# Performance work log

Measured on AMD Instinct MI355X. Metric: run time of the kernel, lower is better.

The kernel has to match this reference:

```python
import jax, jax.numpy as jnp
import numpy as np

EPS = 0.01  # Normalizer eps
N_NODES = 100000
N_EDGES = 1600000


def gcn_conv(x, edge_index, W, b, n_nodes):
    """PyG-style GCNConv: x @ W, symmetric-normalized aggregation with self-loops, + bias."""
    src = jnp.concatenate([edge_index[0], jnp.arange(n_nodes)])  # [E+N]
    dst = jnp.concatenate([edge_index[1], jnp.arange(n_nodes)])  # [E+N]
    h = x @ W  # [N, out]
    ones = jnp.ones_like(dst, dtype=h.dtype)
    deg = jax.ops.segment_sum(ones, dst, num_segments=n_nodes)  # [N]
    dinv = jnp.where(deg > 0, jax.lax.rsqrt(deg), 0.0)
    norm = dinv[src] * dinv[dst]  # [E+N]
    msgs = h[src] * norm[:, None]  # [E+N, out]  (largest intermediate)
    out = jax.ops.segment_sum(msgs, dst, num_segments=n_nodes)  # [N, out]
    return out + b


def setup_inputs() -> dict:
    key = jax.random.key(0)
    k = jax.random.split(key, 6)
    x = jax.random.normal(k[0], (N_NODES, 16), dtype=jnp.float32)
    edge_index = jax.random.randint(k[1], (2, N_EDGES), 0, N_NODES)
    W1 = jax.random.normal(k[2], (16, 64), dtype=jnp.float32) * 0.25
    b1 = jax.random.normal(k[3], (64,), dtype=jnp.float32) * 0.1
    W3 = jax.random.normal(k[4], (64, 32), dtype=jnp.float32) * 0.125
    b3 = jax.random.normal(k[5], (32,), dtype=jnp.float32) * 0.1
    return {"x": x, "edge_index": edge_index, "W1": W1, "b1": b1, "W3": W3, "b3": b3}


def reference(x, edge_index, W1, b1, W3, b3):
    n = x.shape[0]
    h = jax.nn.relu(gcn_conv(x, edge_index, W1, b1, n))
    h = jax.nn.relu(gcn_conv(h, edge_index, W3, b3, n))
    # Normalizer: sequential Welford observe over all nodes then normalize with
    # FINAL stats == population mean / clamped population variance.
    mean = h.mean(axis=0)  # [32]
    var = jnp.maximum(((h - mean) ** 2).mean(axis=0), EPS)  # [32]
    return (h - mean) * jax.lax.rsqrt(var)
```

## Files before the change

### kernel.cpp

```cpp
#include <hip/hip_runtime.h>
#include <hip/hip_fp16.h>

#define EPS 0.01f
#define SCAN_BS 512
#define NCHUNKS 256
#define BUCKET_SHIFT 9
#define BUCKET_SZ (1 << BUCKET_SHIFT)
#define STAGE_CAP 16384


__global__ __launch_bounds__(SCAN_BS) void k_scan_block(const int* __restrict__ in,
                                                        int* __restrict__ out,
                                                        int* __restrict__ bsum, int n) {
    __shared__ int sd[SCAN_BS];
    int t = threadIdx.x;
    int gid = blockIdx.x * SCAN_BS + t;
    int v = (gid < n) ? in[gid] : 0;
    sd[t] = v;
    __syncthreads();
    for (int off = 1; off < SCAN_BS; off <<= 1) {
        int x = (t >= off) ? sd[t - off] : 0;
        __syncthreads();
        sd[t] += x;
        __syncthreads();
    }
    if (gid < n) out[gid] = sd[t] - v;
    if (t == SCAN_BS - 1) bsum[blockIdx.x] = sd[t];
}

__global__ __launch_bounds__(SCAN_BS) void k_scan_tops(int* __restrict__ bsum, int nb) {
    __shared__ int sd[SCAN_BS];
    int t = threadIdx.x;
    int v = (t < nb) ? bsum[t] : 0;
    sd[t] = v;
    __syncthreads();
    for (int off = 1; off < SCAN_BS; off <<= 1) {
        int x = (t >= off) ? sd[t - off] : 0;
        __syncthreads();
        sd[t] += x;
        __syncthreads();
    }
    if (t < nb) bsum[t] = sd[t] - v;
}

__global__ __launch_bounds__(SCAN_BS) void k_scan_add(int* __restrict__ out,
                                                      const int* __restrict__ bsum, int n) {
    int gid = blockIdx.x * SCAN_BS + threadIdx.x;
    if (gid < n) out[gid] += bsum[blockIdx.x];
}


__global__ __launch_bounds__(256) void kA_bucket_hist(const int* __restrict__ dst,
                                                      int* __restrict__ bh, int e,
                                                      int nbuck, int ce) {
    extern __shared__ int hist[];
    int b = blockIdx.x, t = threadIdx.x;
    for (int i = t; i < nbuck; i += 256) hist[i] = 0;
    __syncthreads();
    int lo = b * ce, hi = min(lo + ce, e);
    for (int i = lo + t; i < hi; i += 256) atomicAdd(&hist[dst[i] >> BUCKET_SHIFT], 1);
    __syncthreads();
    for (int i = t; i < nbuck; i += 256) bh[i * NCHUNKS + b] = hist[i];
}

__global__ __launch_bounds__(256) void kC_bucket_scatter(const int* __restrict__ src,
                                                         const int* __restrict__ dst,
                                                         const int* __restrict__ bhs,
                                                         unsigned int* __restrict__ eb, int e,
                                                         int nbuck, int ce) {
    extern __shared__ int cur[];
    int b = blockIdx.x, t = threadIdx.x;
    for (int i = t; i < nbuck; i += 256) cur[i] = bhs[i * NCHUNKS + b];
    __syncthreads();
    int lo = b * ce, hi = min(lo + ce, e);
    for (int i = lo + t; i < hi; i += 256) {
        int s = src[i], d = dst[i];
        int pos = atomicAdd(&cur[d >> BUCKET_SHIFT], 1);
        eb[pos] = ((unsigned int)(d & (BUCKET_SZ - 1)) << 23) | (unsigned int)s;
    }
}

__global__ __launch_bounds__(256) void kDeg_fill_prescale(const unsigned int* __restrict__ eb,
                                                          const int* __restrict__ bhs,
                                                          const float* __restrict__ x,
                                                          int* __restrict__ degi,
                                                          float* __restrict__ dinv,
                                                          int* __restrict__ rowstart,
                                                          int* __restrict__ csr_src,
                                                          __half* __restrict__ xs,
                                                          float* __restrict__ partial,
                                                          int n, int nbuck, int e) {
    __shared__ unsigned int ebs[STAGE_CAP];
    __shared__ int hist[BUCKET_SZ];
    __shared__ int ps[256];
    __shared__ float dv[BUCKET_SZ];
    int k = blockIdx.x, t = threadIdx.x;
    if (k == 0 && t < 64) partial[t] = 0.f;
    for (int i = t; i < BUCKET_SZ; i += 256) hist[i] = 0;
    __syncthreads();
    int lo = bhs[k * NCHUNKS];
    int hi = (k + 1 < nbuck) ? bhs[(k + 1) * NCHUNKS] : e;
    int cnt = hi - lo;
    bool fits = (cnt <= STAGE_CAP);
    for (int i = t; i < cnt; i += 256) {
        unsigned int p = eb[lo + i];
        if (fits) ebs[i] = p;
        atomicAdd(&hist[p >> 23], 1);
    }
    __syncthreads();
    int a0 = hist[2 * t], a1 = hist[2 * t + 1];
    ps[t] = a0 + a1;
    __syncthreads();
    for (int off = 1; off < 256; off <<= 1) {
        int v = (t >= off) ? ps[t - off] : 0;
        __syncthreads();
        ps[t] += v;
        __syncthreads();
    }
    int excl = ps[t] - (a0 + a1);
    int node0 = k << BUCKET_SHIFT;
    int rs0 = lo + excl, rs1 = lo + excl + a0;
    {
        int nd0 = node0 + 2 * t, nd1 = nd0 + 1;
        float d0 = rsqrtf((float)a0 + 1.0f);
        float d1 = rsqrtf((float)a1 + 1.0f);
        dv[2 * t] = d0;
        dv[2 * t + 1] = d1;
        if (nd0 < n) {
            degi[nd0] = a0;
            dinv[nd0] = d0;
            rowstart[nd0] = rs0;
        }
        if (nd1 < n) {
            degi[nd1] = a1;
            dinv[nd1] = d1;
            rowstart[nd1] = rs1;
        }
    }
    __syncthreads();
    hist[2 * t] = rs0;
    hist[2 * t + 1] = rs1;
    {
        const float2* xf2 = (const float2*)x;
        __half2* xs2 = (__half2*)xs;
        for (int i = t; i < BUCKET_SZ * 8; i += 256) {
            int rl = i >> 3;
            int node = node0 + rl;
            if (node < n) {
                float2 vv = xf2[(size_t)node * 8 + (i & 7)];
                float d = dv[rl];
                xs2[(size_t)node * 8 + (i & 7)] = __floats2half2_rn(vv.x * d, vv.y * d);
            }
        }
    }
    __syncthreads();
    for (int i = t; i < cnt; i += 256) {
        unsigned int p = fits ? ebs[i] : eb[lo + i];
        int dl = (int)(p >> 23);
        int s = (int)(p & 0x7fffffu);
        int pos = atomicAdd(&hist[dl], 1);
        csr_src[pos] = s;
    }
}


__global__ __launch_bounds__(256) void k_l1_fused(const int* __restrict__ rowstart,
                                                  const int* __restrict__ degi,
                                                  const int* __restrict__ csr_src,
                                                  const float* __restrict__ dinv,
                                                  const __half* __restrict__ xs,
                                                  const float* __restrict__ W1,
                                                  const float* __restrict__ b1,
                                                  const float* __restrict__ W3,
                                                  __half* __restrict__ h2sA,
                                                  __half* __restrict__ h2sB, int n) {
    __shared__ float w1[16 * 64];
    __shared__ float w3[64 * 32];
    __shared__ float bs[64];
    __shared__ __align__(16) float a[16 * 16];
    __shared__ float z[16 * 64];
    int t = threadIdx.x;
    for (int i = t; i < 16 * 64; i += 256) w1[i] = W1[i];
    for (int i = t; i < 64 * 32; i += 256) w3[i] = W3[i];
    if (t < 64) bs[t] = b1[t];

    int row0 = blockIdx.x * 16;
    int wv = t >> 6;
    int lane = t & 63;
    int c2 = lane & 3;
    int slot = lane >> 2;
    const float2* xf2 = (const float2*)xs;

    for (int nid = 0; nid < 4; ++nid) {
        int node = row0 + wv * 4 + nid;
        if (node < n) {
            const int* sp = csr_src + rowstart[node];
            int deg = degi[node];
            int L = (deg + 15) >> 4;
            int base = slot * L;
            int end = min(base + L, deg);
            __half2 acc0 = __float2half2_rn(0.f), acc1 = acc0;
            for (int k = base; k < end; ++k) {
                int s0 = sp[k];
                float2 raw = xf2[(size_t)s0 * 4 + c2];
                acc0 = __hadd2(acc0, *(const __half2*)&raw.x);
                acc1 = __hadd2(acc1, *(const __half2*)&raw.y);
            }
#pragma unroll
            for (int m = 4; m <= 32; m <<= 1) {
                float o0 = __shfl_xor(*(float*)&acc0, m);
                float o1 = __shfl_xor(*(float*)&acc1, m);
                acc0 = __hadd2(acc0, *(__half2*)&o0);
                acc1 = __hadd2(acc1, *(__half2*)&o1);
            }
            if (slot == 0) {
                float2 lo = __half22float2(acc0), hi = __half22float2(acc1);
                float2 sraw = xf2[(size_t)node * 4 + c2];
                float2 slo = __half22float2(*(const __half2*)&sraw.x);
                float2 shi = __half22float2(*(const __half2*)&sraw.y);
                float dn = dinv[node];
                int r = wv * 4 + nid;
                float4 res;
                res.x = dn * (lo.x + slo.x);
                res.y = dn * (lo.y + slo.y);
                res.z = dn * (hi.x + shi.x);
                res.w = dn * (hi.y + shi.y);
                ((float4*)(a + r * 16))[c2] = res;
            }
        }
    }
    __syncthreads();

    for (int i = t; i < 1024; i += 256) {
        int r = i >> 6, c = i & 63;
        float acc = bs[c];
#pragma unroll
        for (int k = 0; k < 16; ++k) acc += a[r * 16 + k] * w1[k * 64 + c];
        z[i] = acc > 0.f ? acc : 0.f;
    }
    __syncthreads();
    for (int i = t; i < 512; i += 256) {
        int r = i >> 5, c = i & 31;
        float acc = 0.f;
#pragma unroll
        for (int k = 0; k < 64; ++k) acc += z[r * 64 + k] * w3[k * 32 + c];
        int row = row0 + r;
        if (row < n) {
            __half hv = __float2half(acc * dinv[row]);
            if (c < 16) h2sA[(size_t)row * 16 + c] = hv;
            else        h2sB[(size_t)row * 16 + (c - 16)] = hv;
        }
    }
}


__global__ __launch_bounds__(256) void k_gather16x2_stats(const int* __restrict__ rowstart,
                                                          const int* __restrict__ degi,
                                                          const int* __restrict__ csr_src,
                                                          const float* __restrict__ dinv,
                                                          const __half* __restrict__ h2sA,
                                                          const __half* __restrict__ h2sB,
                                                          const float* __restrict__ b3,
                                                          float* __restrict__ out,
                                                          float* __restrict__ partial, int n) {
    int g = blockIdx.x;
    int half = (g >> 2) & 1;
    int nblk = (g >> 3) * 4 + (g & 3);
    int M = (n + 31) >> 5;
    if (nblk >= M) return;
    const float2* h2f = (const float2*)(half ? h2sB : h2sA);
    int col0 = half << 4;
    int t = threadIdx.x;
    int lane = t & 63;
    int c2 = lane & 3;
    int slot = lane >> 2;
    int wv = t >> 6;
    float4 bias = ((const float4*)(b3 + col0))[c2];
    float4 sacc = make_float4(0.f, 0.f, 0.f, 0.f);
    float4 qacc = make_float4(0.f, 0.f, 0.f, 0.f);
    for (int it = 0; it < 8; ++it) {
        int node = nblk * 32 + it * 4 + wv;
        if (node < n) {
            const int* sp = csr_src + rowstart[node];
            int deg = degi[node];
            int L = (deg + 15) >> 4;
            int base = slot * L;
            int end = min(base + L, deg);
            __half2 acc0 = __float2half2_rn(0.f), acc1 = acc0;
            for (int k = base; k < end; ++k) {
                int s0 = sp[k];
                float2 raw = h2f[(size_t)s0 * 4 + c2];
                acc0 = __hadd2(acc0, *(const __half2*)&raw.x);
                acc1 = __hadd2(acc1, *(const __half2*)&raw.y);
            }
#pragma unroll
            for (int m = 4; m <= 32; m <<= 1) {
                float o0 = __shfl_xor(*(float*)&acc0, m);
                float o1 = __shfl_xor(*(float*)&acc1, m);
                acc0 = __hadd2(acc0, *(__half2*)&o0);
                acc1 = __hadd2(acc1, *(__half2*)&o1);
            }
            if (slot == 0) {
                float2 lo = __half22float2(acc0), hi = __half22float2(acc1);
                float2 sraw = h2f[(size_t)node * 4 + c2];
                float2 slo = __half22float2(*(const __half2*)&sraw.x);
                float2 shi = __half22float2(*(const __half2*)&sraw.y);
                float dn = dinv[node];
                float4 v;
                v.x = dn * (lo.x + slo.x) + bias.x;
                v.y = dn * (lo.y + slo.y) + bias.y;
                v.z = dn * (hi.x + shi.x) + bias.z;
                v.w = dn * (hi.y + shi.y) + bias.w;
                v.x = fmaxf(v.x, 0.f);
                v.y = fmaxf(v.y, 0.f);
                v.z = fmaxf(v.z, 0.f);
                v.w = fmaxf(v.w, 0.f);
                ((float4*)(out + (size_t)node * 32 + col0))[c2] = v;
                sacc.x += v.x; sacc.y += v.y; sacc.z += v.z; sacc.w += v.w;
                qacc.x += v.x * v.x; qacc.y += v.y * v.y;
                qacc.z += v.z * v.z; qacc.w += v.w * v.w;
            }
        }
    }
    __shared__ __align__(16) float ls[64], lq[64];
    if (slot == 0) {
        ((float4*)ls)[wv * 4 + c2] = sacc;
        ((float4*)lq)[wv * 4 + c2] = qacc;
    }
    __syncthreads();
    if (t < 16) {
        float a = 0.f, b = 0.f;
#pragma unroll
        for (int w = 0; w < 4; ++w) {
            a += ls[w * 16 + t];
            b += lq[w * 16 + t];
        }
        atomicAdd(&partial[col0 + t], a);
        atomicAdd(&partial[32 + col0 + t], b);
    }
}


__global__ void k_finalize(const float* __restrict__ partial, float* __restrict__ meaninv, int n) {
    int t = threadIdx.x;
    if (t < 32) {
        float invn = 1.0f / (float)n;
        float mean = partial[t] * invn;
        float var = partial[32 + t] * invn - mean * mean;
        var = var > EPS ? var : EPS;
        meaninv[t] = mean;
        meaninv[32 + t] = rsqrtf(var);
    }
}

__global__ void k_norm(float* __restrict__ h, const float* __restrict__ meaninv, int n) {
    int idx = blockIdx.x * blockDim.x + threadIdx.x;
    if (idx < n * 8) {
        int c4 = idx & 7;
        float4 v = ((float4*)h)[idx];
        float4 m = ((const float4*)meaninv)[c4];
        float4 iv = ((const float4*)(meaninv + 32))[c4];
        v.x = (v.x - m.x) * iv.x;
        v.y = (v.y - m.y) * iv.y;
        v.z = (v.z - m.z) * iv.z;
        v.w = (v.w - m.w) * iv.w;
        ((float4*)h)[idx] = v;
    }
}

extern "C" void kernel_launch(void* const* d_in, const int* in_sizes, int n_in,
                              void* d_out, int out_size, void* d_ws, size_t ws_size,
                              hipStream_t stream) {
    const float* x  = (const float*)d_in[0];
    const int* ei   = (const int*)d_in[1];
    const float* W1 = (const float*)d_in[2];
    const float* b1 = (const float*)d_in[3];
    const float* W3 = (const float*)d_in[4];
    const float* b3 = (const float*)d_in[5];

    const int N = in_sizes[0] / 16;
    const int E = in_sizes[1] / 2;
    const int* src = ei;
    const int* dst = ei + E;

    const int NBUCK = (N + BUCKET_SZ - 1) >> BUCKET_SHIFT;
    const int CE = (E + NCHUNKS - 1) / NCHUNKS;
    const int BH_TOTAL = NBUCK * NCHUNKS;

    char* ws = (char*)d_ws;
    int*   degi     = (int*)ws;          ws += (size_t)N * 4;
    float* dinv     = (float*)ws;        ws += (size_t)N * 4;
    int*   rowstart = (int*)ws;          ws += (size_t)N * 4;
    int*   bsum2    = (int*)ws;          ws += (size_t)SCAN_BS * 4;
    int*   bh       = (int*)ws;          ws += (size_t)BH_TOTAL * 4;
    int*   bhs      = (int*)ws;          ws += (size_t)BH_TOTAL * 4;
    unsigned int* eb = (unsigned int*)ws; ws += (size_t)E * 4;
    int*   csr_src  = (int*)ws;          ws += (size_t)E * 4;
    __half* xs      = (__half*)ws;       ws += (size_t)N * 16 * 2;
    __half* h2sA    = (__half*)ws;       ws += (size_t)N * 16 * 2;
    __half* h2sB    = (__half*)ws;       ws += (size_t)N * 16 * 2;
    float* partial  = (float*)ws;        ws += 64 * 4;
    float* meaninv  = (float*)ws;

    float* out = (float*)d_out;

    const int NB2 = (BH_TOTAL + SCAN_BS - 1) / SCAN_BS;

    kA_bucket_hist<<<NCHUNKS, 256, NBUCK * 4, stream>>>(dst, bh, E, NBUCK, CE);
    k_scan_block<<<NB2, SCAN_BS, 0, stream>>>(bh, bhs, bsum2, BH_TOTAL);
    k_scan_tops<<<1, SCAN_BS, 0, stream>>>(bsum2, NB2);
    k_scan_add<<<NB2, SCAN_BS, 0, stream>>>(bhs, bsum2, BH_TOTAL);
    kC_bucket_scatter<<<NCHUNKS, 256, NBUCK * 4, stream>>>(src, dst, bhs, eb, E, NBUCK, CE);

    kDeg_fill_prescale<<<NBUCK, 256, 0, stream>>>(eb, bhs, x, degi, dinv, rowstart,
                                                  csr_src, xs, partial, N, NBUCK, E);

    k_l1_fused<<<(N + 15) / 16, 256, 0, stream>>>(rowstart, degi, csr_src, dinv, xs,
                                                  W1, b1, W3, h2sA, h2sB, N);

    const int M = (N + 31) >> 5;
    const int G = ((M + 3) / 4) * 8;
    k_gather16x2_stats<<<G, 256, 0, stream>>>(rowstart, degi, csr_src, dinv, h2sA, h2sB,
                                              b3, out, partial, N);

    k_finalize<<<1, 64, 0, stream>>>(partial, meaninv, N);
    k_norm<<<(N * 8 + 255) / 256, 256, 0, stream>>>(out, meaninv, N);
}
```

Measured before the change: 191.7 us.

## Batch neighbor gathers across nodes per wave and merge layer-2 column halves

Layer-1 and layer-2 gathers now have each wave process 4 or 8 nodes together. Every lane loads neighbour indices for all of those nodes up front, in a fixed number of unrolled rounds, so many independent loads are in flight instead of one serial loop per node. Accumulation moves from half2 to fp32. The layer-2 features are stored as a single 32-wide half array instead of two 16-wide halves, so one kernel gathers full 64-byte rows rather than launching separate column-half blocks. The cost is higher register pressure from the unrolled per-node accumulators and wasted lanes on low-degree nodes.

```diff
diff --git a/kernel.cpp b/kernel.cpp
--- a/kernel.cpp
+++ b/kernel.cpp
@@ -172,8 +172,7 @@
                                                   const float* __restrict__ W1,
                                                   const float* __restrict__ b1,
                                                   const float* __restrict__ W3,
-                                                  __half* __restrict__ h2sA,
-                                                  __half* __restrict__ h2sB, int n) {
+                                                  __half* __restrict__ h2s, int n) {
     __shared__ float w1[16 * 64];
     __shared__ float w3[64 * 32];
     __shared__ float bs[64];
@@ -187,156 +186,216 @@
     int row0 = blockIdx.x * 16;
     int wv = t >> 6;
     int lane = t & 63;
-    int c2 = lane & 3;
-    int slot = lane >> 2;
+    int g = lane >> 2;
+    int c = lane & 3;
+    int nb = row0 + wv * 4;
     const float2* xf2 = (const float2*)xs;
 
-    for (int nid = 0; nid < 4; ++nid) {
-        int node = row0 + wv * 4 + nid;
-        if (node < n) {
-            const int* sp = csr_src + rowstart[node];
-            int deg = degi[node];
-            int L = (deg + 15) >> 4;
-            int base = slot * L;
-            int end = min(base + L, deg);
-            __half2 acc0 = __float2half2_rn(0.f), acc1 = acc0;
-            for (int k = base; k < end; ++k) {
-                int s0 = sp[k];
-                float2 raw = xf2[(size_t)s0 * 4 + c2];
-                acc0 = __hadd2(acc0, *(const __half2*)&raw.x);
-                acc1 = __hadd2(acc1, *(const __half2*)&raw.y);
+    int rs[4], dg[4];
+#pragma unroll
+    for (int i = 0; i < 4; ++i) {
+        int nd = nb + i;
+        bool ok = nd < n;
+        rs[i] = ok ? rowstart[nd] : 0;
+        dg[i] = ok ? degi[nd] : 0;
+    }
+    float4 acc[4];
+#pragma unroll
+    for (int i = 0; i < 4; ++i) acc[i] = make_float4(0.f, 0.f, 0.f, 0.f);
+
+#pragma unroll
+    for (int r = 0; r < 2; ++r) {
+        int k = r * 16 + g;
+        int idx[4];
+#pragma unroll
+        for (int i = 0; i < 4; ++i) idx[i] = (k < dg[i]) ? csr_src[rs[i] + k] : -1;
+#pragma unroll
+        for (int i = 0; i < 4; ++i) {
+            if (idx[i] >= 0) {
+                float2 raw = xf2[(size_t)idx[i] * 4 + c];
+                float2 lo = __half22float2(*(const __half2*)&raw.x);
+                float2 hi = __half22float2(*(const __half2*)&raw.y);
+                acc[i].x += lo.x; acc[i].y += lo.y;
+                acc[i].z += hi.x; acc[i].w += hi.y;
             }
-#pragma unroll
-            for (int m = 4; m <= 32; m <<= 1) {
-                float o0 = __shfl_xor(*(float*)&acc0, m);
-                float o1 = __shfl_xor(*(float*)&acc1, m);
-                acc0 = __hadd2(acc0, *(__half2*)&o0);
-                acc1 = __hadd2(acc1, *(__half2*)&o1);
+        }
+    }
+#pragma unroll
+    for (int i = 0; i < 4; ++i) {
+        for (int k = 32 + g; k < dg[i]; k += 16) {
+            int s0 = csr_src[rs[i] + k];
+            float2 raw = xf2[(size_t)s0 * 4 + c];
+            float2 lo = __half22float2(*(const __half2*)&raw.x);
+            float2 hi = __half22float2(*(const __half2*)&raw.y);
+            acc[i].x += lo.x; acc[i].y += lo.y;
+            acc[i].z += hi.x; acc[i].w += hi.y;
+        }
+    }
+#pragma unroll
+    for (int i = 0; i < 4; ++i) {
+#pragma unroll
+        for (int m = 4; m <= 32; m <<= 1) {
+            acc[i].x += __shfl_xor(acc[i].x, m);
+            acc[i].y += __shfl_xor(acc[i].y, m);
+            acc[i].z += __shfl_xor(acc[i].z, m);
+            acc[i].w += __shfl_xor(acc[i].w, m);
+        }
+    }
+#pragma unroll
+    for (int i = 0; i < 4; ++i) {
+        int nd = nb + i;
+        if (g == i && nd < n) {
+            float dn = dinv[nd];
+            float2 sraw = xf2[(size_t)nd * 4 + c];
+            float2 slo = __half22float2(*(const __half2*)&sraw.x);
+            float2 shi = __half22float2(*(const __half2*)&sraw.y);
+            float4 res;
+            res.x = dn * (acc[i].x + slo.x);
+            res.y = dn * (acc[i].y + slo.y);
+            res.z = dn * (acc[i].z + shi.x);
+            res.w = dn * (acc[i].w + shi.y);
+            ((float4*)(a + (wv * 4 + i) * 16))[c] = res;
+        }
+    }
+    __syncthreads();
+
+    for (int i = t; i < 1024; i += 256) {
+        int r = i >> 6, cc = i & 63;
+        float acc2 = bs[cc];
+#pragma unroll
+        for (int k = 0; k < 16; ++k) acc2 += a[r * 16 + k] * w1[k * 64 + cc];
+        z[i] = acc2 > 0.f ? acc2 : 0.f;
+    }
+    __syncthreads();
+    for (int i = t; i < 512; i += 256) {
+        int r = i >> 5, cc = i & 31;
+        float acc2 = 0.f;
+#pragma unroll
+        for (int k = 0; k < 64; ++k) acc2 += z[r * 64 + k] * w3[k * 32 + cc];
+        int row = row0 + r;
+        if (row < n) h2s[(size_t)row * 32 + cc] = __float2half(acc2 * dinv[row]);
+    }
+}
+
+
+__global__ __launch_bounds__(256) void k_l2_stats(const int* __restrict__ rowstart,
+                                                  const int* __restrict__ degi,
+                                                  const int* __restrict__ csr_src,
+                                                  const float* __restrict__ dinv,
+                                                  const __half* __restrict__ h2s,
+                                                  const float* __restrict__ b3,
+                                                  float* __restrict__ out,
+                                                  float* __restrict__ partial, int n) {
+    int t = threadIdx.x;
+    int wv = t >> 6;
+    int lane = t & 63;
+    int g = lane >> 3;
+    int c = lane & 7;
+    int nb = blockIdx.x * 32 + wv * 8;
+    const float2* h2f = (const float2*)h2s;
+
+    int rs[8], dg[8];
+#pragma unroll
+    for (int i = 0; i < 8; ++i) {
+        int nd = nb + i;
+        bool ok = nd < n;
+        rs[i] = ok ? rowstart[nd] : 0;
+        dg[i] = ok ? degi[nd] : 0;
+    }
+    float4 acc[8];
+#pragma unroll
+    for (int i = 0; i < 8; ++i) acc[i] = make_float4(0.f, 0.f, 0.f, 0.f);
+
+#pragma unroll
+    for (int r = 0; r < 3; ++r) {
+        int k = r * 8 + g;
+        int idx[8];
+#pragma unroll
+        for (int i = 0; i < 8; ++i) idx[i] = (k < dg[i]) ? csr_src[rs[i] + k] : -1;
+#pragma unroll
+        for (int i = 0; i < 8; ++i) {
+            if (idx[i] >= 0) {
+                float2 raw = h2f[(size_t)idx[i] * 8 + c];
+                float2 lo = __half22float2(*(const __half2*)&raw.x);
+                float2 hi = __half22float2(*(const __half2*)&raw.y);
+                acc[i].x += lo.x; acc[i].y += lo.y;
+                acc[i].z += hi.x; acc[i].w += hi.y;
             }
-            if (slot == 0) {
-                float2 lo = __half22float2(acc0), hi = __half22float2(acc1);
-                float2 sraw = xf2[(size_t)node * 4 + c2];
-                float2 slo = __half22float2(*(const __half2*)&sraw.x);
-                float2 shi = __half22float2(*(const __half2*)&sraw.y);
-                float dn = dinv[node];
-                int r = wv * 4 + nid;
-                float4 res;
-                res.x = dn * (lo.x + slo.x);
-                res.y = dn * (lo.y + slo.y);
-                res.z = dn * (hi.x + shi.x);
-                res.w = dn * (hi.y + shi.y);
-                ((float4*)(a + r * 16))[c2] = res;
-            }
-        }
-    }
-    __syncthreads();
-
-    for (int i = t; i < 1024; i += 256) {
-        int r = i >> 6, c = i & 63;
-        float acc = bs[c];
-#pragma unroll
-        for (int k = 0; k < 16; ++k) acc += a[r * 16 + k] * w1[k * 64 + c];
-        z[i] = acc > 0.f ? acc : 0.f;
-    }
-    __syncthreads();
-    for (int i = t; i < 512; i += 256) {
-        int r = i >> 5, c = i & 31;
-        float acc = 0.f;
-#pragma unroll
-        for (int k = 0; k < 64; ++k) acc += z[r * 64 + k] * w3[k * 32 + c];
-        int row = row0 + r;
-        if (row < n) {
-            __half hv = __float2half(acc * dinv[row]);
-            if (c < 16) h2sA[(size_t)row * 16 + c] = hv;
-            else        h2sB[(size_t)row * 16 + (c - 16)] = hv;
-        }
-    }
-}
-
-
-__global__ __launch_bounds__(256) void k_gather16x2_stats(const int* __restrict__ rowstart,
-                                                          const int* __restrict__ degi,
-                                                          const int* __restrict__ csr_src,
-                                                          const float* __restrict__ dinv,
-                                                          const __half* __restrict__ h2sA,
-                                                          const __half* __restrict__ h2sB,
-                                                          const float* __restrict__ b3,
-                                                          float* __restrict__ out,
-                                                          float* __restrict__ partial, int n) {
-    int g = blockIdx.x;
-    int half = (g >> 2) & 1;
-    int nblk = (g >> 3) * 4 + (g & 3);
-    int M = (n + 31) >> 5;
-    if (nblk >= M) return;
-    const float2* h2f = (const float2*)(half ? h2sB : h2sA);
-    int col0 = half << 4;
-    int t = threadIdx.x;
-    int lane = t & 63;
-    int c2 = lane & 3;
-    int slot = lane >> 2;
-    int wv = t >> 6;
-    float4 bias = ((const float4*)(b3 + col0))[c2];
-    float4 sacc = make_float4(0.f, 0.f, 0.f, 0.f);
-    float4 qacc = make_float4(0.f, 0.f, 0.f, 0.f);
-    for (int it = 0; it < 8; ++it) {
-        int node = nblk * 32 + it * 4 + wv;
-        if (node < n) {
-            const int* sp = csr_src + rowstart[node];
-            int deg = degi[node];
-            int L = (deg + 15) >> 4;
-            int base = slot * L;
-            int end = min(base + L, deg);
-            __half2 acc0 = __float2half2_rn(0.f), acc1 = acc0;
-            for (int k = base; k < end; ++k) {
-                int s0 = sp[k];
-                float2 raw = h2f[(size_t)s0 * 4 + c2];
-                acc0 = __hadd2(acc0, *(const __half2*)&raw.x);
-                acc1 = __hadd2(acc1, *(const __half2*)&raw.y);
-            }
-#pragma unroll
-            for (int m = 4; m <= 32; m <<= 1) {
-                float o0 = __shfl_xor(*(float*)&acc0, m);
-                float o1 = __shfl_xor(*(float*)&acc1, m);
-                acc0 = __hadd2(acc0, *(__half2*)&o0);
-                acc1 = __hadd2(acc1, *(__half2*)&o1);
-            }
-            if (slot == 0) {
-                float2 lo = __half22float2(acc0), hi = __half22float2(acc1);
-                float2 sraw = h2f[(size_t)node * 4 + c2];
-                float2 slo = __half22float2(*(const __half2*)&sraw.x);
-                float2 shi = __half22float2(*(const __half2*)&sraw.y);
-                float dn = dinv[node];
-                float4 v;
-                v.x = dn * (lo.x + slo.x) + bias.x;
-                v.y = dn * (lo.y + slo.y) + bias.y;
-                v.z = dn * (hi.x + shi.x) + bias.z;
-                v.w = dn * (hi.y + shi.y) + bias.w;
-                v.x = fmaxf(v.x, 0.f);
-                v.y = fmaxf(v.y, 0.f);
-                v.z = fmaxf(v.z, 0.f);
-                v.w = fmaxf(v.w, 0.f);
-                ((float4*)(out + (size_t)node * 32 + col0))[c2] = v;
-                sacc.x += v.x; sacc.y += v.y; sacc.z += v.z; sacc.w += v.w;
-                qacc.x += v.x * v.x; qacc.y += v.y * v.y;
-                qacc.z += v.z * v.z; qacc.w += v.w * v.w;
-            }
-        }
-    }
-    __shared__ __align__(16) float ls[64], lq[64];
-    if (slot == 0) {
-        ((float4*)ls)[wv * 4 + c2] = sacc;
-        ((float4*)lq)[wv * 4 + c2] = qacc;
-    }
-    __syncthreads();
-    if (t < 16) {
-        float a = 0.f, b = 0.f;
+        }
+    }
+#pragma unroll
+    for (int i = 0; i < 8; ++i) {
+        for (int k = 24 + g; k < dg[i]; k += 8) {
+            int s0 = csr_src[rs[i] + k];
+            float2 raw = h2f[(size_t)s0 * 8 + c];
+            float2 lo = __half22float2(*(const __half2*)&raw.x);
+            float2 hi = __half22float2(*(const __half2*)&raw.y);
+            acc[i].x += lo.x; acc[i].y += lo.y;
+            acc[i].z += hi.x; acc[i].w += hi.y;
+        }
+    }
+#pragma unroll
+    for (int i = 0; i < 8; ++i) {
+#pragma unroll
+        for (int m = 8; m <= 32; m <<= 1) {
+            acc[i].x += __shfl_xor(acc[i].x, m);
+            acc[i].y += __shfl_xor(acc[i].y, m);
+            acc[i].z += __shfl_xor(acc[i].z, m);
+            acc[i].w += __shfl_xor(acc[i].w, m);
+        }
+    }
+    float4 s4 = make_float4(0.f, 0.f, 0.f, 0.f);
+    float4 q4 = make_float4(0.f, 0.f, 0.f, 0.f);
+    float4 bias = ((const float4*)b3)[c];
+#pragma unroll
+    for (int i = 0; i < 8; ++i) {
+        int nd = nb + i;
+        if (g == i && nd < n) {
+            float dn = dinv[nd];
+            float2 sraw = h2f[(size_t)nd * 8 + c];
+            float2 slo = __half22float2(*(const __half2*)&sraw.x);
+            float2 shi = __half22float2(*(const __half2*)&sraw.y);
+            float4 v;
+            v.x = fmaxf(dn * (acc[i].x + slo.x) + bias.x, 0.f);
+            v.y = fmaxf(dn * (acc[i].y + slo.y) + bias.y, 0.f);
+            v.z = fmaxf(dn * (acc[i].z + shi.x) + bias.z, 0.f);
+            v.w = fmaxf(dn * (acc[i].w + shi.y) + bias.w, 0.f);
+            ((float4*)(out + (size_t)nd * 32))[c] = v;
+            s4.x += v.x; s4.y += v.y; s4.z += v.z; s4.w += v.w;
+            q4.x += v.x * v.x; q4.y += v.y * v.y;
+            q4.z += v.z * v.z; q4.w += v.w * v.w;
+        }
+    }
+#pragma unroll
+    for (int m = 8; m <= 32; m <<= 1) {
+        s4.x += __shfl_xor(s4.x, m); s4.y += __shfl_xor(s4.y, m);
+        s4.z += __shfl_xor(s4.z, m); s4.w += __shfl_xor(s4.w, m);
+        q4.x += __shfl_xor(q4.x, m); q4.y += __shfl_xor(q4.y, m);
+        q4.z += __shfl_xor(q4.z, m); q4.w += __shfl_xor(q4.w, m);
+    }
+    __shared__ __align__(16) float4 lsv[32], lqv[32];
+    if (g == 0) {
+        lsv[wv * 8 + c] = s4;
+        lqv[wv * 8 + c] = q4;
+    }
+    __syncthreads();
+    if (t < 8) {
+        float4 a2 = make_float4(0.f, 0.f, 0.f, 0.f);
+        float4 b2 = make_float4(0.f, 0.f, 0.f, 0.f);
 #pragma unroll
         for (int w = 0; w < 4; ++w) {
-            a += ls[w * 16 + t];
-            b += lq[w * 16 + t];
-        }
-        atomicAdd(&partial[col0 + t], a);
-        atomicAdd(&partial[32 + col0 + t], b);
+            float4 sv = lsv[w * 8 + t], qv = lqv[w * 8 + t];
+            a2.x += sv.x; a2.y += sv.y; a2.z += sv.z; a2.w += sv.w;
+            b2.x += qv.x; b2.y += qv.y; b2.z += qv.z; b2.w += qv.w;
+        }
+        atomicAdd(&partial[4 * t + 0], a2.x);
+        atomicAdd(&partial[4 * t + 1], a2.y);
+        atomicAdd(&partial[4 * t + 2], a2.z);
+        atomicAdd(&partial[4 * t + 3], a2.w);
+        atomicAdd(&partial[32 + 4 * t + 0], b2.x);
+        atomicAdd(&partial[32 + 4 * t + 1], b2.y);
+        atomicAdd(&partial[32 + 4 * t + 2], b2.z);
+        atomicAdd(&partial[32 + 4 * t + 3], b2.w);
     }
 }
 
@@ -397,8 +456,7 @@
     unsigned int* eb = (unsigned int*)ws; ws += (size_t)E * 4;
     int*   csr_src  = (int*)ws;          ws += (size_t)E * 4;
     __half* xs      = (__half*)ws;       ws += (size_t)N * 16 * 2;
-    __half* h2sA    = (__half*)ws;       ws += (size_t)N * 16 * 2;
-    __half* h2sB    = (__half*)ws;       ws += (size_t)N * 16 * 2;
+    __half* h2s     = (__half*)ws;       ws += (size_t)N * 32 * 2;
     float* partial  = (float*)ws;        ws += 64 * 4;
     float* meaninv  = (float*)ws;
 
@@ -416,12 +474,10 @@
                                                   csr_src, xs, partial, N, NBUCK, E);
 
     k_l1_fused<<<(N + 15) / 16, 256, 0, stream>>>(rowstart, degi, csr_src, dinv, xs,
-                                                  W1, b1, W3, h2sA, h2sB, N);
-
-    const int M = (N + 31) >> 5;
-    const int G = ((M + 3) / 4) * 8;
-    k_gather16x2_stats<<<G, 256, 0, stream>>>(rowstart, degi, csr_src, dinv, h2sA, h2sB,
-                                              b3, out, partial, N);
+                                                  W1, b1, W3, h2s, N);
+
+    k_l2_stats<<<(N + 31) / 32, 256, 0, stream>>>(rowstart, degi, csr_src, dinv, h2s,
+                                                  b3, out, partial, N);
 
     k_finalize<<<1, 64, 0, stream>>>(partial, meaninv, N);
     k_norm<<<(N * 8 + 255) / 256, 256, 0, stream>>>(out, meaninv, N);
```

Result: slower. 298.9 us (+55.9%).
